# Kernel optimization log

Hardware: AMD Instinct MI355X
Metric: run time of the kernel (lower is better)

## Reference

```python
import jax, jax.numpy as jnp
import numpy as np

LMAX = 4
NCOEF = (LMAX + 1) ** 2  # 25 spherical-harmonic coefficients
EXPAND = np.repeat(np.arange(LMAX + 1), [2 * l + 1 for l in range(LMAX + 1)])  # per-l -> per-(l,m)
N, E, C, H, HEADS, ACH, VCH, F, G, DE, AEMB, MAXEL = 10000, 50000, 64, 64, 8, 16, 8, 128, 36, 32, 32, 100


def setup_inputs() -> dict:
    ks = jax.random.split(jax.random.key(0), 24)
    f = lambda i, shape, s=1.0: jax.random.normal(ks[i], shape, jnp.float32) * s
    return dict(
        x=f(0, (N, NCOEF, C)),
        edge_index=jax.random.randint(ks[1], (2, E), 0, N),
        atomic_numbers=jax.random.randint(ks[2], (N,), 0, MAXEL),
        edge_distance=jax.random.uniform(ks[3], (E, DE), jnp.float32),
        wigner=f(4, (E, NCOEF, NCOEF), 0.2),
        src_tab=f(5, (MAXEL, AEMB), 0.02), tgt_tab=f(6, (MAXEL, AEMB), 0.02),
        rad_w1=f(7, (DE + 2 * AEMB, 64), 0.1), rad_b1=jnp.zeros((64,), jnp.float32),
        rad_w2=f(8, (64, 64), 0.1), rad_b2=jnp.zeros((64,), jnp.float32),
        rad_w3=f(9, (64, (LMAX + 1) * 2 * C), 0.05), rad_b3=jnp.ones(((LMAX + 1) * 2 * C,), jnp.float32),
        W1=f(10, (2 * C, H), 0.05), W0_extra=f(11, (2 * C, HEADS * ACH + H), 0.05),
        alpha_dot=f(12, (HEADS, ACH), 0.1),
        to_grid=f(13, (G, NCOEF), 0.2), from_grid=f(14, (NCOEF, G), 0.2),
        proj_out=f(15, (HEADS * VCH, C), 0.1),
        gamma1=jnp.ones((C,), jnp.float32), gamma2=jnp.ones((C,), jnp.float32),
        gl_w=f(16, (C, F), 0.1), gl_b=jnp.zeros((F,), jnp.float32),
        ffn_w1=f(17, (C, F), 0.1), ffn_b1=jnp.zeros((F,), jnp.float32),
        ffn_w2=f(18, (F, C), 0.1), ffn_b2=jnp.zeros((C,), jnp.float32),
    )


def _rmsnorm(x, gamma, eps=1e-6):
    # equivariant norm over the coefficient axis, per node/channel
    rms = jnp.sqrt(jnp.mean(x * x, axis=1, keepdims=True) + eps)  # [N,1,C]
    return x / rms * gamma


def _s2_sep_act(gate, x, to_grid, from_grid):
    # separable S2 activation: scalars = silu(gating scalars); l>0 via grid SiLU
    grid = jnp.einsum('gi,nih->ngh', to_grid, x)
    xg = jnp.einsum('ig,ngh->nih', from_grid, jax.nn.silu(grid))
    return jnp.concatenate([jax.nn.silu(gate)[:, None, :], xg[:, 1:, :]], axis=1)


def reference(x, edge_index, atomic_numbers, edge_distance, wigner, src_tab, tgt_tab,
              rad_w1, rad_b1, rad_w2, rad_b2, rad_w3, rad_b3,
              W1, W0_extra, alpha_dot, to_grid, from_grid, proj_out,
              gamma1, gamma2, gl_w, gl_b, ffn_w1, ffn_b1, ffn_w2, ffn_b2):
    src, dst = edge_index[0], edge_index[1]
    # ---- SO2 equivariant graph attention (gather -> rotate -> conv -> act -> attn -> scatter) ----
    h = _rmsnorm(x, gamma1)
    xe = jnp.concatenate([h[src], h[dst]], axis=-1)          # [E,25,2C] edge gather
    xe = jnp.einsum('eij,ejc->eic', wigner, xe)              # rotate into edge frame
    ef = jnp.concatenate([edge_distance, src_tab[atomic_numbers[src]],
                          tgt_tab[atomic_numbers[dst]]], axis=-1)
    r = jax.nn.silu(ef @ rad_w1 + rad_b1)
    r = jax.nn.silu(r @ rad_w2 + rad_b2)
    r = (r @ rad_w3 + rad_b3).reshape(-1, LMAX + 1, 2 * C)[:, EXPAND, :]  # m-shared radial, [E,25,2C]
    xe = xe * r
    extra = xe[:, 0, :] @ W0_extra                           # extra m=0 channels
    alpha_f = extra[:, :HEADS * ACH].reshape(-1, HEADS, ACH)
    gate = extra[:, HEADS * ACH:]                            # [E,H]
    msg = jnp.einsum('eic,ch->eih', xe, W1)                  # [E,25,H]
    msg = _s2_sep_act(gate, msg, to_grid, from_grid)
    # attention weights: softmax over incoming edges of each destination node
    alpha = jnp.einsum('eha,ha->eh', jax.nn.silu(alpha_f), alpha_dot)
    amax = jax.lax.stop_gradient(jax.ops.segment_max(alpha, dst, num_segments=N))
    a = jnp.exp(alpha - amax[dst])
    a = a / (jax.ops.segment_sum(a, dst, num_segments=N)[dst] + 1e-8)
    msg = (msg.reshape(-1, NCOEF, HEADS, VCH) * a[:, None, :, None]).reshape(-1, NCOEF, HEADS * VCH)
    msg = jnp.einsum('eji,ejc->eic', wigner, msg)            # rotate back (D^T)
    agg = jax.ops.segment_sum(msg, dst, num_segments=N)      # scatter-add, [N,25,H]
    x = x + agg @ proj_out
    # ---- feed-forward with separable S2 activation ----
    h = _rmsnorm(x, gamma2)
    gate = h[:, 0, :] @ gl_w + gl_b
    f1 = jnp.einsum('nic,cf->nif', h, ffn_w1)
    f1 = jnp.concatenate([f1[:, :1, :] + ffn_b1, f1[:, 1:, :]], axis=1)  # bias on l=0 only
    f1 = _s2_sep_act(gate, f1, to_grid, from_grid)
    f2 = jnp.einsum('nif,fc->nic', f1, ffn_w2)
    f2 = jnp.concatenate([f2[:, :1, :] + ffn_b2, f2[:, 1:, :]], axis=1)
    return x + f2
```

## Files before the change

kernel.cpp:

```cpp
#include <hip/hip_runtime.h>
#include <hip/hip_bf16.h>

#define NN 10000
#define NE 50000
#define MAXDEG 32

typedef __attribute__((ext_vector_type(8))) short bfrag8;
typedef __attribute__((ext_vector_type(4))) short s16x4;
typedef __attribute__((ext_vector_type(8))) short s16x8;
typedef __attribute__((ext_vector_type(4))) float f32x4;

__device__ __forceinline__ float silu_f(float v){ return v / (1.0f + __expf(-v)); }
__device__ __forceinline__ short f2b(float f){
  unsigned u = __float_as_uint(f);
  u += 0x7fffu + ((u>>16)&1u);
  return (short)(u>>16);
}
__device__ __forceinline__ float b2f(short s){
  return __uint_as_float(((unsigned)(unsigned short)s)<<16);
}
__device__ __forceinline__ void gload_lds16(const void* g, void* l){
  __builtin_amdgcn_global_load_lds(
      (const __attribute__((address_space(1))) void*)g,
      (__attribute__((address_space(3))) void*)l, 16, 0, 0);
}

__global__ __launch_bounds__(256) void k_rms1(const float* __restrict__ x,
                                              const float* __restrict__ gamma,
                                              short* __restrict__ hT){
  int idx = blockIdx.x*256 + threadIdx.x;
  if (idx >= NN*64) return;
  int n = idx>>6, c = idx&63;
  const float* xp = x + (size_t)n*1600 + c;
  float v[25]; float ss = 0.f;
#pragma unroll
  for (int i=0;i<25;i++){ v[i] = xp[i*64]; ss += v[i]*v[i]; }
  float inv = gamma[c] * rsqrtf(ss*(1.f/25.f) + 1e-6f);
  short* hp = hT + (size_t)n*2048 + c*32;
  const int sw = (c>>1)&3;
#pragma unroll
  for (int s=0;s<4;s++){
    s16x8 o;
#pragma unroll
    for (int k=0;k<8;k++){
      int j = s*8 + k;
      o[k] = (j<25) ? f2b(v[j]*inv) : (short)0;
    }
    *(s16x8*)(hp + ((s ^ sw)<<3)) = o;
  }
}

__global__ void k_wprep(const float* __restrict__ W1, const float* __restrict__ tog,
                        const float* __restrict__ fromg, const float* __restrict__ proj,
                        const float* __restrict__ fw1, const float* __restrict__ fw2,
                        const float* __restrict__ rw1, const float* __restrict__ rw2,
                        const float* __restrict__ rw3, const float* __restrict__ w0e,
                        short* __restrict__ w1t, short* __restrict__ togA,
                        short* __restrict__ fgA, short* __restrict__ projT,
                        short* __restrict__ fw1T, short* __restrict__ fw2T,
                        short* __restrict__ rw1T, short* __restrict__ rw2T,
                        short* __restrict__ rw3T, short* __restrict__ w0eT){
  int t0 = blockIdx.x*blockDim.x + threadIdx.x;
  int stride = gridDim.x*blockDim.x;
  for (int idx=t0; idx<64*136; idx+=stride){
    int hh = idx/136, k = idx-136*hh;
    w1t[idx] = (k<128) ? f2b(W1[k*64+hh]) : (short)0;
  }
  for (int idx=t0; idx<48*40; idx+=stride){
    int g = idx/40, i = idx-40*g;
    togA[idx] = (g<36 && i<25) ? f2b(tog[g*25+i]) : (short)0;
  }
  for (int idx=t0; idx<32*72; idx+=stride){
    int j = idx/72, g = idx-72*j;
    fgA[idx] = (j<25 && g<36) ? f2b(fromg[j*36+g]) : (short)0;
  }
  for (int idx=t0; idx<64*64; idx+=stride){
    int c = idx>>6, k = idx&63;
    projT[idx] = f2b(proj[k*64+c]);
  }
  for (int idx=t0; idx<128*64; idx+=stride){
    int f = idx>>6, c = idx&63;
    fw1T[idx] = f2b(fw1[c*128+f]);
  }
  for (int idx=t0; idx<64*128; idx+=stride){
    int c = idx>>7, f = idx&127;
    fw2T[idx] = f2b(fw2[f*64+c]);
  }
  for (int idx=t0; idx<64*96; idx+=stride){
    int n = idx/96, k = idx-96*n;
    rw1T[idx] = f2b(rw1[k*64+n]);
  }
  for (int idx=t0; idx<64*64; idx+=stride){
    int n = idx>>6, k = idx&63;
    rw2T[idx] = f2b(rw2[k*64+n]);
  }
  for (int idx=t0; idx<640*64; idx+=stride){
    int n = idx>>6, k = idx&63;
    rw3T[idx] = f2b(rw3[(size_t)k*640+n]);
  }
  for (int idx=t0; idx<192*128; idx+=stride){
    int m = idx>>7, c = idx&127;
    w0eT[idx] = f2b(w0e[c*192+m]);
  }
}

__global__ __launch_bounds__(256) void k_fill(const int* __restrict__ ei,
                                              int* __restrict__ cnt,
                                              unsigned short* __restrict__ eidTab){
  int e = blockIdx.x*256 + threadIdx.x;
  if (e >= NE) return;
  int dst = ei[NE+e];
  int pos = atomicAdd(&cnt[dst], 1);
  if (pos < MAXDEG) eidTab[dst*MAXDEG + pos] = (unsigned short)e;
}

__global__ __launch_bounds__(256) void k_scan(const int* __restrict__ cnt,
                                              int* __restrict__ pref){
  __shared__ int ts[256];
  int tid = threadIdx.x;
  int base = tid*40;
  int s = 0;
  for (int k=0;k<40;k++){ int i = base+k; if (i<NN) s += min(cnt[i],MAXDEG); }
  ts[tid] = s;
  __syncthreads();
  if (tid==0){ int run=0; for(int t=0;t<256;t++){ int v=ts[t]; ts[t]=run; run+=v; } }
  __syncthreads();
  int run = ts[tid];
  for (int k=0;k<40;k++){
    int i = base+k;
    if (i<NN){ pref[i]=run; run += min(cnt[i],MAXDEG); }
  }
}

__global__ __launch_bounds__(256) void k_compact(const int* __restrict__ cnt,
                                                 const int* __restrict__ pref,
                                                 const unsigned short* __restrict__ eidTab,
                                                 int* __restrict__ order){
  int idx = blockIdx.x*256 + threadIdx.x;
  if (idx >= NN*MAXDEG) return;
  int n = idx>>5, k = idx&31;
  if (k < min(cnt[n],MAXDEG)) order[pref[n]+k] = (int)eidTab[n*MAXDEG+k];
}

__global__ __launch_bounds__(256,4) void k_radial(
  const int* __restrict__ ei, const int* __restrict__ an,
  const float* __restrict__ edist,
  const float* __restrict__ stab, const float* __restrict__ ttab,
  const short* __restrict__ rw1T, const float* __restrict__ rb1,
  const short* __restrict__ rw2T, const float* __restrict__ rb2,
  const short* __restrict__ rw3T, const float* __restrict__ rb3,
  short* __restrict__ rfS)
{
  __shared__ __align__(16) short SP[7936];
  const int tid = threadIdx.x;
  const int wv = tid>>6, lane = tid&63, lo = lane&15, q = lane>>4;
  const int e0 = blockIdx.x*32;
  {
    int e = tid>>3;
    int ee = min(e0+e, NE-1);
    int srcE = ei[ee], dstE = ei[NE+ee];
    const float* dp = edist + (size_t)ee*32;
    const float* sp = stab + (size_t)an[srcE]*32;
    const float* tp = ttab + (size_t)an[dstE]*32;
    int kb = tid&7;
#pragma unroll
    for (int it=0; it<12; ++it){
      int k = kb + it*8;
      float v = (k<32) ? dp[k] : (k<64 ? sp[k-32] : tp[k-64]);
      SP[e*104+k] = f2b(v);
    }
  }
  __syncthreads();
  {
    f32x4 zf={0.f,0.f,0.f,0.f}; f32x4 acc[2]={zf,zf};
#pragma unroll
    for (int kt=0;kt<3;kt++){
      bfrag8 a = *(const bfrag8*)&rw1T[(wv*16+lo)*96 + kt*32 + q*8];
#pragma unroll
      for (int et=0;et<2;et++){
        bfrag8 b = *(const bfrag8*)&SP[(et*16+lo)*104 + kt*32 + q*8];
        acc[et] = __builtin_amdgcn_mfma_f32_16x16x32_bf16(a,b,acc[et],0,0,0);
      }
    }
    int n1 = wv*16 + q*4;
    const float4 bb = *(const float4*)&rb1[n1];
#pragma unroll
    for (int et=0;et<2;et++){
      s16x4 o;
      o[0]=f2b(silu_f(acc[et][0]+bb.x)); o[1]=f2b(silu_f(acc[et][1]+bb.y));
      o[2]=f2b(silu_f(acc[et][2]+bb.z)); o[3]=f2b(silu_f(acc[et][3]+bb.w));
      *(s16x4*)&SP[3328 + (et*16+lo)*72 + n1] = o;
    }
  }
  __syncthreads();
  {
    f32x4 zf={0.f,0.f,0.f,0.f}; f32x4 acc[2]={zf,zf};
#pragma unroll
    for (int kt=0;kt<2;kt++){
      bfrag8 a = *(const bfrag8*)&rw2T[(wv*16+lo)*64 + kt*32 + q*8];
#pragma unroll
      for (int et=0;et<2;et++){
        bfrag8 b = *(const bfrag8*)&SP[3328 + (et*16+lo)*72 + kt*32 + q*8];
        acc[et] = __builtin_amdgcn_mfma_f32_16x16x32_bf16(a,b,acc[et],0,0,0);
      }
    }
    int n2 = wv*16 + q*4;
    const float4 bb = *(const float4*)&rb2[n2];
#pragma unroll
    for (int et=0;et<2;et++){
      s16x4 o;
      o[0]=f2b(silu_f(acc[et][0]+bb.x)); o[1]=f2b(silu_f(acc[et][1]+bb.y));
      o[2]=f2b(silu_f(acc[et][2]+bb.z)); o[3]=f2b(silu_f(acc[et][3]+bb.w));
      *(s16x4*)&SP[5632 + (et*16+lo)*72 + n2] = o;
    }
  }
  __syncthreads();
  {
    bfrag8 bfr[2][2];
#pragma unroll
    for (int et=0;et<2;et++)
#pragma unroll
      for (int kt=0;kt<2;kt++)
        bfr[et][kt] = *(const bfrag8*)&SP[5632 + (et*16+lo)*72 + kt*32 + q*8];
    for (int mi=0; mi<10; ++mi){
      int n3base = (wv + mi*4)*16;
      f32x4 zf={0.f,0.f,0.f,0.f}; f32x4 acc[2]={zf,zf};
#pragma unroll
      for (int kt=0;kt<2;kt++){
        bfrag8 a = *(const bfrag8*)&rw3T[(size_t)(n3base+lo)*64 + kt*32 + q*8];
        acc[0] = __builtin_amdgcn_mfma_f32_16x16x32_bf16(a,bfr[0][kt],acc[0],0,0,0);
        acc[1] = __builtin_amdgcn_mfma_f32_16x16x32_bf16(a,bfr[1][kt],acc[1],0,0,0);
      }
      int n3 = n3base + q*4;
      const float4 bb = *(const float4*)&rb3[n3];
#pragma unroll
      for (int et=0;et<2;et++){
        int e = e0 + et*16 + lo;
        if (e < NE){
          s16x4 o;
          o[0]=f2b(acc[et][0]+bb.x); o[1]=f2b(acc[et][1]+bb.y);
          o[2]=f2b(acc[et][2]+bb.z); o[3]=f2b(acc[et][3]+bb.w);
          *(s16x4*)&rfS[(size_t)e*640 + n3] = o;
        }
      }
    }
  }
}

__global__ __launch_bounds__(256,8) void k_edge(
  const short* __restrict__ hT, const int* __restrict__ ei,
  const int* __restrict__ order, const float* __restrict__ wig,
  const short* __restrict__ w1t, const short* __restrict__ togA,
  const short* __restrict__ fgA, const short* __restrict__ w0eT,
  const float* __restrict__ adot,
  const short* __restrict__ rfS, float* __restrict__ asum,
  float* __restrict__ agg)
{
  __shared__ __align__(16) short SH[7312];
  float* gateL = (float*)&SH[7168];
  float* ahead = (float*)&SH[7296];
  const int tid = threadIdx.x;
  const int wv = tid>>6, lane = tid&63, lo = lane&15, q = lane>>4;
  const int bid = blockIdx.x;
  const int e = order[(bid&7)*(NE/8) + (bid>>3)];
  const int src = ei[e], dst = ei[NE+e];

  {
    const char* g0 = (const char*)(hT + (size_t)src*2048) + wv*1024 + lane*16;
    const char* g1 = (const char*)(hT + (size_t)dst*2048) + wv*1024 + lane*16;
    gload_lds16(g0, (char*)SH + wv*1024);
    gload_lds16(g1, (char*)SH + 4096 + wv*1024);
  }
  {
    const s16x4 z4 = {0,0,0,0};
    if (tid < 128) *(s16x4*)&SH[4096 + tid*4] = z4;
  }
  const float* w = wig + (size_t)e*625;
  const bfrag8 wz = {0,0,0,0,0,0,0,0};
  bfrag8 wb0, wtb0, wb1 = wz, wtb1 = wz;
#pragma unroll
  for (int m=0;m<8;m++){
    int j = q*8+m;
    float v0  = (j<25) ? w[lo*25+j] : 0.f;
    float vt0 = (j<25) ? w[j*25+lo] : 0.f;
    wb0[m]  = f2b(v0);
    wtb0[m] = f2b(vt0);
  }
  if (lo < 9){
#pragma unroll
    for (int m=0;m<8;m++){
      int j = q*8+m;
      float v1  = (j<25) ? w[(16+lo)*25+j]  : 0.f;
      float vt1 = (j<25) ? w[j*25+16+lo]    : 0.f;
      wb1[m]  = f2b(v1);
      wtb1[m] = f2b(vt1);
    }
  }
  s16x4 rvp[2][2];
  {
    const short* rrow = rfS + (size_t)e*640;
#pragma unroll
    for (int t=0;t<2;t++){
      int c0 = (2*wv+t)*16 + q*4;
#pragma unroll
      for (int nt=0;nt<2;nt++){
        int i = nt*16 + lo;
        int l = (i>=16)?4:((i>=9)?3:((i>=4)?2:((i>=1)?1:0)));
        rvp[t][nt] = *(const s16x4*)&rrow[l*128 + c0];
      }
    }
  }
  asm volatile("s_waitcnt vmcnt(0)" ::: "memory");
  __syncthreads();

  f32x4 xacc[2][2];
  {
    const f32x4 zf = {0.f,0.f,0.f,0.f};
#pragma unroll
    for (int t=0;t<2;t++){
      int c = (2*wv+t)*16 + lo;
      bfrag8 a = *(const bfrag8*)&SH[c*32 + ((q ^ ((c>>1)&3))<<3)];
      xacc[t][0] = __builtin_amdgcn_mfma_f32_16x16x32_bf16(a, wb0, zf, 0,0,0);
      xacc[t][1] = __builtin_amdgcn_mfma_f32_16x16x32_bf16(a, wb1, zf, 0,0,0);
    }
  }
  __syncthreads();
#pragma unroll
  for (int t=0;t<2;t++){
    int c0 = (2*wv+t)*16 + q*4;
#pragma unroll
    for (int nt=0;nt<2;nt++){
      int i = nt*16 + lo;
      s16x4 rv = rvp[t][nt];
      s16x4 o;
#pragma unroll
      for (int r=0;r<4;r++) o[r] = f2b(xacc[t][nt][r]*b2f(rv[r]));
      *(s16x4*)&SH[i*136 + c0] = o;
    }
  }
  __syncthreads();

  {
    bfrag8 xb[4];
#pragma unroll
    for (int kt=0;kt<4;kt++) xb[kt] = *(const bfrag8*)&SH[kt*32 + q*8];
    const f32x4 zf = {0.f,0.f,0.f,0.f};
#pragma unroll
    for (int t=0;t<3;t++){
      const int mt = wv*3 + t;
      f32x4 acc = zf;
#pragma unroll
      for (int kt=0;kt<4;kt++){
        bfrag8 a = *(const bfrag8*)&w0eT[(mt*16+lo)*128 + kt*32 + q*8];
        acc = __builtin_amdgcn_mfma_f32_16x16x32_bf16(a, xb[kt], acc, 0,0,0);
      }
      if (mt < 8){
        float s = 0.f;
#pragma unroll
        for (int r=0;r<4;r++) s += silu_f(acc[r]) * adot[mt*16 + q*4 + r];
        s += __shfl_xor(s, 16);
        s += __shfl_xor(s, 32);
        float eh = __expf(s);
        if (lane==0){
          ahead[mt] = eh;
          unsafeAtomicAdd(&asum[(size_t)dst*8 + mt], eh);
        }
      } else if (lo==0){
        int g0 = mt*16 - 128 + q*4;
#pragma unroll
        for (int r=0;r<4;r++) gateL[g0+r] = silu_f(acc[r]);
      }
    }
  }
  {
    const int hh = wv*16 + lo;
    const f32x4 zf = {0.f,0.f,0.f,0.f};
    f32x4 acc[2] = {zf,zf};
#pragma unroll
    for (int kt=0;kt<4;kt++){
      bfrag8 b = *(const bfrag8*)&w1t[hh*136 + kt*32 + q*8];
#pragma unroll
      for (int t=0;t<2;t++){
        bfrag8 a = *(const bfrag8*)&SH[(t*16+lo)*136 + kt*32 + q*8];
        acc[t] = __builtin_amdgcn_mfma_f32_16x16x32_bf16(a, b, acc[t], 0,0,0);
      }
    }
#pragma unroll
    for (int t=0;t<2;t++){
      s16x4 o;
#pragma unroll
      for (int r=0;r<4;r++) o[r] = f2b(acc[t][r]);
      *(s16x4*)&SH[4608 + hh*40 + t*16 + q*4] = o;
    }
  }
  __syncthreads();

  {
    const int hh = wv*16 + lo;
    bfrag8 b = *(const bfrag8*)&SH[4608 + hh*40 + q*8];
    const f32x4 zf = {0.f,0.f,0.f,0.f};
    f32x4 acc[3] = {zf,zf,zf};
#pragma unroll
    for (int t=0;t<3;t++){
      bfrag8 a = *(const bfrag8*)&togA[(t*16+lo)*40 + q*8];
      acc[t] = __builtin_amdgcn_mfma_f32_16x16x32_bf16(a, b, acc[t], 0,0,0);
    }
#pragma unroll
    for (int t=0;t<3;t++){
      s16x4 o;
#pragma unroll
      for (int r=0;r<4;r++) o[r] = f2b(silu_f(acc[t][r]));
      *(s16x4*)&SH[hh*72 + t*16 + q*4] = o;
    }
  }
  {
    const int hh = wv*16 + lo;
    const f32x4 zf = {0.f,0.f,0.f,0.f};
    f32x4 acc[2] = {zf,zf};
#pragma unroll
    for (int kt=0;kt<2;kt++){
      bfrag8 b = *(const bfrag8*)&SH[hh*72 + kt*32 + q*8];
#pragma unroll
      for (int t=0;t<2;t++){
        bfrag8 a = *(const bfrag8*)&fgA[(t*16+lo)*72 + kt*32 + q*8];
        acc[t] = __builtin_amdgcn_mfma_f32_16x16x32_bf16(a, b, acc[t], 0,0,0);
      }
    }
    float ah = ahead[hh>>3];
#pragma unroll
    for (int t=0;t<2;t++){
      s16x4 o;
#pragma unroll
      for (int r=0;r<4;r++){
        int j = t*16 + q*4 + r;
        float v = (j==0) ? gateL[hh] : acc[t][r];
        o[r] = f2b(v*ah);
      }
      *(s16x4*)&SH[4608 + hh*40 + t*16 + q*4] = o;
    }
  }
  {
    const int hh = wv*16 + lo;
    bfrag8 b = *(const bfrag8*)&SH[4608 + hh*40 + q*8];
    const f32x4 zf = {0.f,0.f,0.f,0.f};
    f32x4 acc0 = __builtin_amdgcn_mfma_f32_16x16x32_bf16(wtb0, b, zf, 0,0,0);
    f32x4 acc1 = __builtin_amdgcn_mfma_f32_16x16x32_bf16(wtb1, b, zf, 0,0,0);
    float* aggp = agg + (size_t)dst*1600;
#pragma unroll
    for (int r=0;r<4;r++){
      int i0 = q*4 + r;
      unsafeAtomicAdd(&aggp[i0*64 + hh], acc0[r]);
      int i1 = 16 + q*4 + r;
      if (i1 < 25) unsafeAtomicAdd(&aggp[i1*64 + hh], acc1[r]);
    }
  }
}

__global__ __launch_bounds__(256,4) void k_node(
  const float* __restrict__ x, const float* __restrict__ aggin,
  const float* __restrict__ asum,
  const short* __restrict__ projT, const float* __restrict__ gamma2,
  const float* __restrict__ glw, const float* __restrict__ glb,
  const short* __restrict__ fw1T, const float* __restrict__ fb1,
  const short* __restrict__ fw2T, const float* __restrict__ fb2,
  const short* __restrict__ togA, const short* __restrict__ fgA,
  float* __restrict__ out)
{
  __shared__ __align__(16) short P[19072];
  float* xF    = (float*)P;
  short* sgB   = P + 4352;
  short* hh2B  = P + 4352;
  short* f1B   = P + 13568;
  short* aggB  = P + 13568;
  short* xgB   = P + 13568;
  float* invc  = ((float*)P) + 9344;
  float* gateF = ((float*)P) + 9408;
  const int tid = threadIdx.x;
  const int wv = tid>>6, lane = tid&63, lo = lane&15, q = lane>>4;
  const int n = blockIdx.x;
  const s16x4 z4 = {0,0,0,0};

  for (int idx=tid; idx<400; idx+=256){
    int i = idx>>4, k = idx&15;
    float sc = 1.f/(asum[(size_t)n*8 + (k>>1)] + 1e-8f);
    const float4 v = *(const float4*)(aggin + (size_t)n*1600 + (size_t)idx*4);
    s16x4 o; o[0]=f2b(v.x*sc); o[1]=f2b(v.y*sc); o[2]=f2b(v.z*sc); o[3]=f2b(v.w*sc);
    *(s16x4*)&aggB[i*72 + k*4] = o;
  }
  for (int idx=tid; idx<126; idx+=256)
    *(s16x4*)&hh2B[25*72 + idx*4] = z4;
  for (int idx=tid; idx<512; idx+=256){
    int f = idx>>2, gg = 48 + (idx&3)*4;
    *(s16x4*)&sgB[f*72 + gg] = z4;
  }
  __syncthreads();

  {
    f32x4 zf={0.f,0.f,0.f,0.f}; f32x4 acc[2]={zf,zf};
    const int c = wv*16 + lo;
#pragma unroll
    for (int kt=0;kt<2;kt++){
      bfrag8 b = *(const bfrag8*)&projT[c*64 + kt*32 + q*8];
#pragma unroll
      for (int t=0;t<2;t++){
        bfrag8 a = *(const bfrag8*)&aggB[(t*16+lo)*72 + kt*32 + q*8];
        acc[t] = __builtin_amdgcn_mfma_f32_16x16x32_bf16(a,b,acc[t],0,0,0);
      }
    }
#pragma unroll
    for (int t=0;t<2;t++)
#pragma unroll
      for (int r=0;r<4;r++){
        int i = t*16 + q*4 + r;
        if (i<25) xF[i*68+c] = acc[t][r] + x[(size_t)n*1600 + i*64 + c];
      }
  }
  __syncthreads();
  if (tid<64){
    float ss=0.f;
#pragma unroll
    for (int i=0;i<25;i++){ float v = xF[i*68+tid]; ss += v*v; }
    invc[tid] = gamma2[tid]*rsqrtf(ss*(1.f/25.f)+1e-6f);
  }
  __syncthreads();
  for (int idx=tid; idx<1600; idx+=256){
    int i=idx>>6, c=idx&63;
    hh2B[i*72+c] = f2b(xF[i*68+c]*invc[c]);
  }
  if (tid<128){
    float a = glb[tid];
#pragma unroll 8
    for (int c=0;c<64;c++) a += xF[c]*invc[c]*glw[c*128+tid];
    gateF[tid] = silu_f(a);
  }
  __syncthreads();

  {
    f32x4 zf={0.f,0.f,0.f,0.f}; f32x4 acc[2][2]={{zf,zf},{zf,zf}};
#pragma unroll
    for (int kt=0;kt<2;kt++){
      bfrag8 a0 = *(const bfrag8*)&hh2B[(lo)*72 + kt*32 + q*8];
      bfrag8 a1 = *(const bfrag8*)&hh2B[(16+lo)*72 + kt*32 + q*8];
#pragma unroll
      for (int s=0;s<2;s++){
        int f = wv*32 + s*16 + lo;
        bfrag8 b = *(const bfrag8*)&fw1T[f*64 + kt*32 + q*8];
        acc[0][s] = __builtin_amdgcn_mfma_f32_16x16x32_bf16(a0,b,acc[0][s],0,0,0);
        acc[1][s] = __builtin_amdgcn_mfma_f32_16x16x32_bf16(a1,b,acc[1][s],0,0,0);
      }
    }
#pragma unroll
    for (int s=0;s<2;s++){
      int f = wv*32 + s*16 + lo;
      float bb = fb1[f];
#pragma unroll
      for (int t=0;t<2;t++){
        s16x4 o;
#pragma unroll
        for (int r=0;r<4;r++){
          int i = t*16+q*4+r;
          o[r] = f2b(acc[t][s][r] + (i==0 ? bb : 0.f));
        }
        *(s16x4*)&f1B[f*40 + t*16 + q*4] = o;
      }
    }
  }
  __syncthreads();

  {
    f32x4 zf={0.f,0.f,0.f,0.f}; f32x4 acc[3][2]={{zf,zf},{zf,zf},{zf,zf}};
    bfrag8 a0 = *(const bfrag8*)&togA[(lo)*40 + q*8];
    bfrag8 a1 = *(const bfrag8*)&togA[(16+lo)*40 + q*8];
    bfrag8 a2 = *(const bfrag8*)&togA[(32+lo)*40 + q*8];
#pragma unroll
    for (int s=0;s<2;s++){
      int f = wv*32 + s*16 + lo;
      bfrag8 b = *(const bfrag8*)&f1B[f*40 + q*8];
      acc[0][s] = __builtin_amdgcn_mfma_f32_16x16x32_bf16(a0,b,acc[0][s],0,0,0);
      acc[1][s] = __builtin_amdgcn_mfma_f32_16x16x32_bf16(a1,b,acc[1][s],0,0,0);
      acc[2][s] = __builtin_amdgcn_mfma_f32_16x16x32_bf16(a2,b,acc[2][s],0,0,0);
    }
#pragma unroll
    for (int s=0;s<2;s++){
      int f = wv*32 + s*16 + lo;
#pragma unroll
      for (int t=0;t<3;t++){
        s16x4 o;
#pragma unroll
        for (int r=0;r<4;r++) o[r] = f2b(silu_f(acc[t][s][r]));
        *(s16x4*)&sgB[f*72 + t*16 + q*4] = o;
      }
    }
  }
  __syncthreads();

  {
    f32x4 zf={0.f,0.f,0.f,0.f}; f32x4 acc[2][2]={{zf,zf},{zf,zf}};
#pragma unroll
    for (int kt=0;kt<2;kt++){
#pragma unroll
      for (int t=0;t<2;t++){
        bfrag8 b = *(const bfrag8*)&fgA[(t*16+lo)*72 + kt*32 + q*8];
#pragma unroll
        for (int s=0;s<2;s++){
          bfrag8 a = *(const bfrag8*)&sgB[(wv*32+s*16+lo)*72 + kt*32 + q*8];
          acc[s][t] = __builtin_amdgcn_mfma_f32_16x16x32_bf16(a,b,acc[s][t],0,0,0);
        }
      }
    }
#pragma unroll
    for (int s=0;s<2;s++){
      int f0 = wv*32 + s*16 + q*4;
#pragma unroll
      for (int t=0;t<2;t++){
        int j = t*16 + lo;
        s16x4 o;
#pragma unroll
        for (int r=0;r<4;r++)
          o[r] = f2b(j==0 ? gateF[f0+r] : acc[s][t][r]);
        *(s16x4*)&xgB[j*136 + f0] = o;
      }
    }
  }
  __syncthreads();

  {
    f32x4 zf={0.f,0.f,0.f,0.f}; f32x4 acc[2]={zf,zf};
    const int c = wv*16 + lo;
#pragma unroll
    for (int kt=0;kt<4;kt++){
      bfrag8 b = *(const bfrag8*)&fw2T[c*128 + kt*32 + q*8];
#pragma unroll
      for (int t=0;t<2;t++){
        bfrag8 a = *(const bfrag8*)&xgB[(t*16+lo)*136 + kt*32 + q*8];
        acc[t] = __builtin_amdgcn_mfma_f32_16x16x32_bf16(a,b,acc[t],0,0,0);
      }
    }
    float bb = fb2[c];
#pragma unroll
    for (int t=0;t<2;t++)
#pragma unroll
      for (int r=0;r<4;r++){
        int i = t*16 + q*4 + r;
        if (i<25)
          out[(size_t)n*1600 + i*64 + c] = xF[i*68+c] + acc[t][r] + (i==0 ? bb : 0.f);
      }
  }
}

extern "C" void kernel_launch(void* const* d_in, const int* in_sizes, int n_in,
                              void* d_out, int out_size, void* d_ws, size_t ws_size,
                              hipStream_t stream) {
  (void)in_sizes; (void)n_in; (void)ws_size;
  const float* x     = (const float*)d_in[0];
  const int*   ei    = (const int*)d_in[1];
  const int*   an    = (const int*)d_in[2];
  const float* edist = (const float*)d_in[3];
  const float* wig   = (const float*)d_in[4];
  const float* stab  = (const float*)d_in[5];
  const float* ttab  = (const float*)d_in[6];
  const float* rw1   = (const float*)d_in[7];
  const float* rb1   = (const float*)d_in[8];
  const float* rw2   = (const float*)d_in[9];
  const float* rb2   = (const float*)d_in[10];
  const float* rw3   = (const float*)d_in[11];
  const float* rb3   = (const float*)d_in[12];
  const float* W1    = (const float*)d_in[13];
  const float* w0e   = (const float*)d_in[14];
  const float* adot  = (const float*)d_in[15];
  const float* tog   = (const float*)d_in[16];
  const float* fromg = (const float*)d_in[17];
  const float* proj  = (const float*)d_in[18];
  const float* g1    = (const float*)d_in[19];
  const float* g2    = (const float*)d_in[20];
  const float* glw   = (const float*)d_in[21];
  const float* glb   = (const float*)d_in[22];
  const float* fw1   = (const float*)d_in[23];
  const float* fb1   = (const float*)d_in[24];
  const float* fw2   = (const float*)d_in[25];
  const float* fb2   = (const float*)d_in[26];
  float* out = (float*)d_out;

  char* wsb = (char*)d_ws;
  short* hT     = (short*)(wsb);
  short* rfS    = (short*)(wsb + 40960000);
  float* asum   = (float*)(wsb + 104960000);
  int*   cnt    = (int*)(wsb + 105280000);
  int*   pref   = (int*)(wsb + 105320000);
  int*   order  = (int*)(wsb + 105360000);
  unsigned short* eidTab = (unsigned short*)(wsb + 105560000);
  short* w1t    = (short*)(wsb + 106200000);
  short* togA   = (short*)(wsb + 106217408);
  short* fgA    = (short*)(wsb + 106221248);
  short* projT  = (short*)(wsb + 106225856);
  short* fw1T   = (short*)(wsb + 106234048);
  short* fw2T   = (short*)(wsb + 106250432);
  short* rw1T   = (short*)(wsb + 106266816);
  short* rw2T   = (short*)(wsb + 106279104);
  short* rw3T   = (short*)(wsb + 106287296);
  short* w0eT   = (short*)(wsb + 106369216);

  hipMemsetAsync(asum, 0, (size_t)NN*8*sizeof(float), stream);
  hipMemsetAsync(cnt, 0, (size_t)NN*sizeof(int), stream);
  hipMemsetAsync(d_out, 0, (size_t)out_size*sizeof(float), stream);

  k_wprep<<<32, 256, 0, stream>>>(W1, tog, fromg, proj, fw1, fw2, rw1, rw2, rw3, w0e,
                                  w1t, togA, fgA, projT, fw1T, fw2T,
                                  rw1T, rw2T, rw3T, w0eT);
  k_fill   <<<(NE+255)/256, 256, 0, stream>>>(ei, cnt, eidTab);
  k_scan   <<<1, 256, 0, stream>>>(cnt, pref);
  k_compact<<<(NN*MAXDEG+255)/256, 256, 0, stream>>>(cnt, pref, eidTab, order);
  k_rms1  <<<(NN*64+255)/256, 256, 0, stream>>>(x, g1, hT);
  k_radial<<<(NE+31)/32, 256, 0, stream>>>(ei, an, edist, stab, ttab,
                                           rw1T, rb1, rw2T, rb2, rw3T, rb3, rfS);
  k_edge  <<<NE, 256, 0, stream>>>(hT, ei, order, wig, w1t, togA, fgA, w0eT, adot,
                                   rfS, asum, out);
  k_node  <<<NN, 256, 0, stream>>>(x, out, asum, projT, g2, glw, glb,
                                   fw1T, fb1, fw2T, fb2, togA, fgA, out);
}
```

Baseline: 1.083 ms.

## Process edges per destination node to replace atomic scatter with register accumulation

The edge kernel now launches one block per destination node and loops serially over that node's incoming edges from the bucket table. It accumulates the rotated messages in MFMA registers and the softmax denominators in LDS, then writes each aggregate row once with normalization applied. This drops the scan and compact kernels, the output and softmax-sum memsets, and all global float atomics. In exchange, the per-edge work inside each block is serialized with several barriers per edge. The dst row load is now shared across edges, and load imbalance across nodes of different degree becomes possible. Occupancy is reduced to 6 blocks because of the larger LDS footprint.

Result: slower. 1.280 ms (+18.1%).

```diff
diff --git a/kernel.cpp b/kernel.cpp
--- a/kernel.cpp
+++ b/kernel.cpp
@@ -114,34 +114,6 @@
   if (pos < MAXDEG) eidTab[dst*MAXDEG + pos] = (unsigned short)e;
 }
 
-__global__ __launch_bounds__(256) void k_scan(const int* __restrict__ cnt,
-                                              int* __restrict__ pref){
-  __shared__ int ts[256];
-  int tid = threadIdx.x;
-  int base = tid*40;
-  int s = 0;
-  for (int k=0;k<40;k++){ int i = base+k; if (i<NN) s += min(cnt[i],MAXDEG); }
-  ts[tid] = s;
-  __syncthreads();
-  if (tid==0){ int run=0; for(int t=0;t<256;t++){ int v=ts[t]; ts[t]=run; run+=v; } }
-  __syncthreads();
-  int run = ts[tid];
-  for (int k=0;k<40;k++){
-    int i = base+k;
-    if (i<NN){ pref[i]=run; run += min(cnt[i],MAXDEG); }
-  }
-}
-
-__global__ __launch_bounds__(256) void k_compact(const int* __restrict__ cnt,
-                                                 const int* __restrict__ pref,
-                                                 const unsigned short* __restrict__ eidTab,
-                                                 int* __restrict__ order){
-  int idx = blockIdx.x*256 + threadIdx.x;
-  if (idx >= NN*MAXDEG) return;
-  int n = idx>>5, k = idx&31;
-  if (k < min(cnt[n],MAXDEG)) order[pref[n]+k] = (int)eidTab[n*MAXDEG+k];
-}
-
 __global__ __launch_bounds__(256,4) void k_radial(
   const int* __restrict__ ei, const int* __restrict__ an,
   const float* __restrict__ edist,
@@ -247,218 +219,229 @@
   }
 }
 
-__global__ __launch_bounds__(256,8) void k_edge(
+__global__ __launch_bounds__(256,6) void k_edge(
   const short* __restrict__ hT, const int* __restrict__ ei,
-  const int* __restrict__ order, const float* __restrict__ wig,
+  const float* __restrict__ wig,
+  const int* __restrict__ cnt, const unsigned short* __restrict__ eidTab,
   const short* __restrict__ w1t, const short* __restrict__ togA,
   const short* __restrict__ fgA, const short* __restrict__ w0eT,
   const float* __restrict__ adot,
-  const short* __restrict__ rfS, float* __restrict__ asum,
-  float* __restrict__ agg)
+  const short* __restrict__ rfS, float* __restrict__ agg)
 {
-  __shared__ __align__(16) short SH[7312];
-  float* gateL = (float*)&SH[7168];
-  float* ahead = (float*)&SH[7296];
+  __shared__ __align__(16) short SH[11424];
+  float* wigL  = (float*)&SH[8704];
+  float* gateL = (float*)&SH[11264];
+  float* ahead = (float*)&SH[11392];
+  float* dsum  = (float*)&SH[11408];
   const int tid = threadIdx.x;
   const int wv = tid>>6, lane = tid&63, lo = lane&15, q = lane>>4;
-  const int bid = blockIdx.x;
-  const int e = order[(bid&7)*(NE/8) + (bid>>3)];
-  const int src = ei[e], dst = ei[NE+e];
-
-  {
-    const char* g0 = (const char*)(hT + (size_t)src*2048) + wv*1024 + lane*16;
-    const char* g1 = (const char*)(hT + (size_t)dst*2048) + wv*1024 + lane*16;
-    gload_lds16(g0, (char*)SH + wv*1024);
-    gload_lds16(g1, (char*)SH + 4096 + wv*1024);
-  }
+  const int n = blockIdx.x;
+  const int deg = min(cnt[n], MAXDEG);
+  const bfrag8 wz = {0,0,0,0,0,0,0,0};
+
   {
     const s16x4 z4 = {0,0,0,0};
-    if (tid < 128) *(s16x4*)&SH[4096 + tid*4] = z4;
-  }
-  const float* w = wig + (size_t)e*625;
-  const bfrag8 wz = {0,0,0,0,0,0,0,0};
-  bfrag8 wb0, wtb0, wb1 = wz, wtb1 = wz;
-#pragma unroll
-  for (int m=0;m<8;m++){
-    int j = q*8+m;
-    float v0  = (j<25) ? w[lo*25+j] : 0.f;
-    float vt0 = (j<25) ? w[j*25+lo] : 0.f;
-    wb0[m]  = f2b(v0);
-    wtb0[m] = f2b(vt0);
-  }
-  if (lo < 9){
+    for (int idx=tid; idx<1152; idx+=256) *(s16x4*)&SH[4096 + idx*4] = z4;
+    if (tid < 8) dsum[tid] = 0.f;
+  }
+  gload_lds16((const char*)(hT + (size_t)n*2048) + wv*1024 + lane*16,
+              (char*)SH + 4096 + wv*1024);
+
+  f32x4 aca0 = {0.f,0.f,0.f,0.f}, aca1 = {0.f,0.f,0.f,0.f};
+
+  for (int k=0; k<deg; ++k){
+    const int e = (int)eidTab[n*MAXDEG + k];
+    const int src = ei[e];
+    gload_lds16((const char*)(hT + (size_t)src*2048) + wv*1024 + lane*16,
+                (char*)SH + wv*1024);
+    {
+      const float* w = wig + (size_t)e*625;
+      for (int idx=tid; idx<625; idx+=256) wigL[idx] = w[idx];
+    }
+    s16x4 rvp[2][2];
+    {
+      const short* rrow = rfS + (size_t)e*640;
+#pragma unroll
+      for (int t=0;t<2;t++){
+        int c0 = (2*wv+t)*16 + q*4;
+#pragma unroll
+        for (int nt=0;nt<2;nt++){
+          int i = nt*16 + lo;
+          int l = (i>=16)?4:((i>=9)?3:((i>=4)?2:((i>=1)?1:0)));
+          rvp[t][nt] = *(const s16x4*)&rrow[l*128 + c0];
+        }
+      }
+    }
+    asm volatile("s_waitcnt vmcnt(0)" ::: "memory");
+    __syncthreads();
+
+    bfrag8 wb0, wtb0, wb1 = wz, wtb1 = wz;
 #pragma unroll
     for (int m=0;m<8;m++){
       int j = q*8+m;
-      float v1  = (j<25) ? w[(16+lo)*25+j]  : 0.f;
-      float vt1 = (j<25) ? w[j*25+16+lo]    : 0.f;
-      wb1[m]  = f2b(v1);
-      wtb1[m] = f2b(vt1);
-    }
-  }
-  s16x4 rvp[2][2];
-  {
-    const short* rrow = rfS + (size_t)e*640;
+      wb0[m]  = (j<25) ? f2b(wigL[lo*25+j]) : (short)0;
+      wtb0[m] = (j<25) ? f2b(wigL[j*25+lo]) : (short)0;
+    }
+    if (lo < 9){
+#pragma unroll
+      for (int m=0;m<8;m++){
+        int j = q*8+m;
+        wb1[m]  = (j<25) ? f2b(wigL[(16+lo)*25+j]) : (short)0;
+        wtb1[m] = (j<25) ? f2b(wigL[j*25+16+lo])   : (short)0;
+      }
+    }
+    f32x4 xacc[2][2];
+    {
+      const f32x4 zf = {0.f,0.f,0.f,0.f};
+#pragma unroll
+      for (int t=0;t<2;t++){
+        int c = (2*wv+t)*16 + lo;
+        bfrag8 a = *(const bfrag8*)&SH[c*32 + ((q ^ ((c>>1)&3))<<3)];
+        xacc[t][0] = __builtin_amdgcn_mfma_f32_16x16x32_bf16(a, wb0, zf, 0,0,0);
+        xacc[t][1] = __builtin_amdgcn_mfma_f32_16x16x32_bf16(a, wb1, zf, 0,0,0);
+      }
+    }
+    __syncthreads();
 #pragma unroll
     for (int t=0;t<2;t++){
       int c0 = (2*wv+t)*16 + q*4;
 #pragma unroll
       for (int nt=0;nt<2;nt++){
         int i = nt*16 + lo;
-        int l = (i>=16)?4:((i>=9)?3:((i>=4)?2:((i>=1)?1:0)));
-        rvp[t][nt] = *(const s16x4*)&rrow[l*128 + c0];
-      }
-    }
-  }
-  asm volatile("s_waitcnt vmcnt(0)" ::: "memory");
-  __syncthreads();
-
-  f32x4 xacc[2][2];
-  {
-    const f32x4 zf = {0.f,0.f,0.f,0.f};
-#pragma unroll
-    for (int t=0;t<2;t++){
-      int c = (2*wv+t)*16 + lo;
-      bfrag8 a = *(const bfrag8*)&SH[c*32 + ((q ^ ((c>>1)&3))<<3)];
-      xacc[t][0] = __builtin_amdgcn_mfma_f32_16x16x32_bf16(a, wb0, zf, 0,0,0);
-      xacc[t][1] = __builtin_amdgcn_mfma_f32_16x16x32_bf16(a, wb1, zf, 0,0,0);
-    }
-  }
-  __syncthreads();
-#pragma unroll
-  for (int t=0;t<2;t++){
-    int c0 = (2*wv+t)*16 + q*4;
-#pragma unroll
-    for (int nt=0;nt<2;nt++){
-      int i = nt*16 + lo;
-      s16x4 rv = rvp[t][nt];
-      s16x4 o;
-#pragma unroll
-      for (int r=0;r<4;r++) o[r] = f2b(xacc[t][nt][r]*b2f(rv[r]));
-      *(s16x4*)&SH[i*136 + c0] = o;
-    }
-  }
-  __syncthreads();
-
-  {
-    bfrag8 xb[4];
-#pragma unroll
-    for (int kt=0;kt<4;kt++) xb[kt] = *(const bfrag8*)&SH[kt*32 + q*8];
-    const f32x4 zf = {0.f,0.f,0.f,0.f};
-#pragma unroll
-    for (int t=0;t<3;t++){
-      const int mt = wv*3 + t;
-      f32x4 acc = zf;
+        s16x4 rv = rvp[t][nt];
+        s16x4 o;
+#pragma unroll
+        for (int r=0;r<4;r++) o[r] = f2b(xacc[t][nt][r]*b2f(rv[r]));
+        *(s16x4*)&SH[4096 + i*136 + c0] = o;
+      }
+    }
+    __syncthreads();
+
+    {
+      bfrag8 xb[4];
+#pragma unroll
+      for (int kt=0;kt<4;kt++) xb[kt] = *(const bfrag8*)&SH[4096 + kt*32 + q*8];
+      const f32x4 zf = {0.f,0.f,0.f,0.f};
+#pragma unroll
+      for (int t=0;t<3;t++){
+        const int mt = wv*3 + t;
+        f32x4 acc = zf;
+#pragma unroll
+        for (int kt=0;kt<4;kt++){
+          bfrag8 a = *(const bfrag8*)&w0eT[(mt*16+lo)*128 + kt*32 + q*8];
+          acc = __builtin_amdgcn_mfma_f32_16x16x32_bf16(a, xb[kt], acc, 0,0,0);
+        }
+        if (mt < 8){
+          float s = 0.f;
+#pragma unroll
+          for (int r=0;r<4;r++) s += silu_f(acc[r]) * adot[mt*16 + q*4 + r];
+          s += __shfl_xor(s, 16);
+          s += __shfl_xor(s, 32);
+          float eh = __expf(s);
+          if (lane==0){
+            ahead[mt] = eh;
+            dsum[mt] += eh;
+          }
+        } else if (lo==0){
+          int g0 = mt*16 - 128 + q*4;
+#pragma unroll
+          for (int r=0;r<4;r++) gateL[g0+r] = silu_f(acc[r]);
+        }
+      }
+    }
+    {
+      const int hh = wv*16 + lo;
+      const f32x4 zf = {0.f,0.f,0.f,0.f};
+      f32x4 acc[2] = {zf,zf};
 #pragma unroll
       for (int kt=0;kt<4;kt++){
-        bfrag8 a = *(const bfrag8*)&w0eT[(mt*16+lo)*128 + kt*32 + q*8];
-        acc = __builtin_amdgcn_mfma_f32_16x16x32_bf16(a, xb[kt], acc, 0,0,0);
-      }
-      if (mt < 8){
-        float s = 0.f;
-#pragma unroll
-        for (int r=0;r<4;r++) s += silu_f(acc[r]) * adot[mt*16 + q*4 + r];
-        s += __shfl_xor(s, 16);
-        s += __shfl_xor(s, 32);
-        float eh = __expf(s);
-        if (lane==0){
-          ahead[mt] = eh;
-          unsafeAtomicAdd(&asum[(size_t)dst*8 + mt], eh);
-        }
-      } else if (lo==0){
-        int g0 = mt*16 - 128 + q*4;
-#pragma unroll
-        for (int r=0;r<4;r++) gateL[g0+r] = silu_f(acc[r]);
-      }
-    }
-  }
+        bfrag8 b = *(const bfrag8*)&w1t[hh*136 + kt*32 + q*8];
+#pragma unroll
+        for (int t=0;t<2;t++){
+          bfrag8 a = *(const bfrag8*)&SH[4096 + (t*16+lo)*136 + kt*32 + q*8];
+          acc[t] = __builtin_amdgcn_mfma_f32_16x16x32_bf16(a, b, acc[t], 0,0,0);
+        }
+      }
+#pragma unroll
+      for (int t=0;t<2;t++){
+        s16x4 o;
+#pragma unroll
+        for (int r=0;r<4;r++) o[r] = f2b(acc[t][r]);
+        *(s16x4*)&SH[8704 + hh*40 + t*16 + q*4] = o;
+      }
+    }
+    __syncthreads();
+
+    {
+      const int hh = wv*16 + lo;
+      bfrag8 b = *(const bfrag8*)&SH[8704 + hh*40 + q*8];
+      const f32x4 zf = {0.f,0.f,0.f,0.f};
+      f32x4 acc[3] = {zf,zf,zf};
+#pragma unroll
+      for (int t=0;t<3;t++){
+        bfrag8 a = *(const bfrag8*)&togA[(t*16+lo)*40 + q*8];
+        acc[t] = __builtin_amdgcn_mfma_f32_16x16x32_bf16(a, b, acc[t], 0,0,0);
+      }
+#pragma unroll
+      for (int t=0;t<3;t++){
+        s16x4 o;
+#pragma unroll
+        for (int r=0;r<4;r++) o[r] = f2b(silu_f(acc[t][r]));
+        *(s16x4*)&SH[4096 + hh*72 + t*16 + q*4] = o;
+      }
+    }
+    {
+      const int hh = wv*16 + lo;
+      const f32x4 zf = {0.f,0.f,0.f,0.f};
+      f32x4 acc[2] = {zf,zf};
+#pragma unroll
+      for (int kt=0;kt<2;kt++){
+        bfrag8 b = *(const bfrag8*)&SH[4096 + hh*72 + kt*32 + q*8];
+#pragma unroll
+        for (int t=0;t<2;t++){
+          bfrag8 a = *(const bfrag8*)&fgA[(t*16+lo)*72 + kt*32 + q*8];
+          acc[t] = __builtin_amdgcn_mfma_f32_16x16x32_bf16(a, b, acc[t], 0,0,0);
+        }
+      }
+      float ah = ahead[hh>>3];
+#pragma unroll
+      for (int t=0;t<2;t++){
+        s16x4 o;
+#pragma unroll
+        for (int r=0;r<4;r++){
+          int j = t*16 + q*4 + r;
+          float v = (j==0) ? gateL[hh] : acc[t][r];
+          o[r] = f2b(v*ah);
+        }
+        *(s16x4*)&SH[8704 + hh*40 + t*16 + q*4] = o;
+      }
+    }
+    {
+      const int hh = wv*16 + lo;
+      bfrag8 b = *(const bfrag8*)&SH[8704 + hh*40 + q*8];
+      aca0 = __builtin_amdgcn_mfma_f32_16x16x32_bf16(wtb0, b, aca0, 0,0,0);
+      aca1 = __builtin_amdgcn_mfma_f32_16x16x32_bf16(wtb1, b, aca1, 0,0,0);
+    }
+    __syncthreads();
+  }
+
+  __syncthreads();
   {
     const int hh = wv*16 + lo;
-    const f32x4 zf = {0.f,0.f,0.f,0.f};
-    f32x4 acc[2] = {zf,zf};
-#pragma unroll
-    for (int kt=0;kt<4;kt++){
-      bfrag8 b = *(const bfrag8*)&w1t[hh*136 + kt*32 + q*8];
-#pragma unroll
-      for (int t=0;t<2;t++){
-        bfrag8 a = *(const bfrag8*)&SH[(t*16+lo)*136 + kt*32 + q*8];
-        acc[t] = __builtin_amdgcn_mfma_f32_16x16x32_bf16(a, b, acc[t], 0,0,0);
-      }
-    }
-#pragma unroll
-    for (int t=0;t<2;t++){
-      s16x4 o;
-#pragma unroll
-      for (int r=0;r<4;r++) o[r] = f2b(acc[t][r]);
-      *(s16x4*)&SH[4608 + hh*40 + t*16 + q*4] = o;
-    }
-  }
-  __syncthreads();
-
-  {
-    const int hh = wv*16 + lo;
-    bfrag8 b = *(const bfrag8*)&SH[4608 + hh*40 + q*8];
-    const f32x4 zf = {0.f,0.f,0.f,0.f};
-    f32x4 acc[3] = {zf,zf,zf};
-#pragma unroll
-    for (int t=0;t<3;t++){
-      bfrag8 a = *(const bfrag8*)&togA[(t*16+lo)*40 + q*8];
-      acc[t] = __builtin_amdgcn_mfma_f32_16x16x32_bf16(a, b, acc[t], 0,0,0);
-    }
-#pragma unroll
-    for (int t=0;t<3;t++){
-      s16x4 o;
-#pragma unroll
-      for (int r=0;r<4;r++) o[r] = f2b(silu_f(acc[t][r]));
-      *(s16x4*)&SH[hh*72 + t*16 + q*4] = o;
-    }
-  }
-  {
-    const int hh = wv*16 + lo;
-    const f32x4 zf = {0.f,0.f,0.f,0.f};
-    f32x4 acc[2] = {zf,zf};
-#pragma unroll
-    for (int kt=0;kt<2;kt++){
-      bfrag8 b = *(const bfrag8*)&SH[hh*72 + kt*32 + q*8];
-#pragma unroll
-      for (int t=0;t<2;t++){
-        bfrag8 a = *(const bfrag8*)&fgA[(t*16+lo)*72 + kt*32 + q*8];
-        acc[t] = __builtin_amdgcn_mfma_f32_16x16x32_bf16(a, b, acc[t], 0,0,0);
-      }
-    }
-    float ah = ahead[hh>>3];
-#pragma unroll
-    for (int t=0;t<2;t++){
-      s16x4 o;
-#pragma unroll
-      for (int r=0;r<4;r++){
-        int j = t*16 + q*4 + r;
-        float v = (j==0) ? gateL[hh] : acc[t][r];
-        o[r] = f2b(v*ah);
-      }
-      *(s16x4*)&SH[4608 + hh*40 + t*16 + q*4] = o;
-    }
-  }
-  {
-    const int hh = wv*16 + lo;
-    bfrag8 b = *(const bfrag8*)&SH[4608 + hh*40 + q*8];
-    const f32x4 zf = {0.f,0.f,0.f,0.f};
-    f32x4 acc0 = __builtin_amdgcn_mfma_f32_16x16x32_bf16(wtb0, b, zf, 0,0,0);
-    f32x4 acc1 = __builtin_amdgcn_mfma_f32_16x16x32_bf16(wtb1, b, zf, 0,0,0);
-    float* aggp = agg + (size_t)dst*1600;
+    float sc = 1.f/(dsum[hh>>3] + 1e-8f);
+    float* aggp = agg + (size_t)n*1600;
 #pragma unroll
     for (int r=0;r<4;r++){
       int i0 = q*4 + r;
-      unsafeAtomicAdd(&aggp[i0*64 + hh], acc0[r]);
+      aggp[i0*64 + hh] = aca0[r]*sc;
       int i1 = 16 + q*4 + r;
-      if (i1 < 25) unsafeAtomicAdd(&aggp[i1*64 + hh], acc1[r]);
+      if (i1 < 25) aggp[i1*64 + hh] = aca1[r]*sc;
     }
   }
 }
 
 __global__ __launch_bounds__(256,4) void k_node(
   const float* __restrict__ x, const float* __restrict__ aggin,
-  const float* __restrict__ asum,
   const short* __restrict__ projT, const float* __restrict__ gamma2,
   const float* __restrict__ glw, const float* __restrict__ glb,
   const short* __restrict__ fw1T, const float* __restrict__ fb1,
@@ -482,9 +465,8 @@
 
   for (int idx=tid; idx<400; idx+=256){
     int i = idx>>4, k = idx&15;
-    float sc = 1.f/(asum[(size_t)n*8 + (k>>1)] + 1e-8f);
     const float4 v = *(const float4*)(aggin + (size_t)n*1600 + (size_t)idx*4);
-    s16x4 o; o[0]=f2b(v.x*sc); o[1]=f2b(v.y*sc); o[2]=f2b(v.z*sc); o[3]=f2b(v.w*sc);
+    s16x4 o; o[0]=f2b(v.x); o[1]=f2b(v.y); o[2]=f2b(v.z); o[3]=f2b(v.w);
     *(s16x4*)&aggB[i*72 + k*4] = o;
   }
   for (int idx=tid; idx<126; idx+=256)
@@ -651,7 +633,7 @@
 extern "C" void kernel_launch(void* const* d_in, const int* in_sizes, int n_in,
                               void* d_out, int out_size, void* d_ws, size_t ws_size,
                               hipStream_t stream) {
-  (void)in_sizes; (void)n_in; (void)ws_size;
+  (void)in_sizes; (void)n_in; (void)ws_size; (void)out_size;
   const float* x     = (const float*)d_in[0];
   const int*   ei    = (const int*)d_in[1];
   const int*   an    = (const int*)d_in[2];
@@ -684,37 +666,30 @@
   char* wsb = (char*)d_ws;
   short* hT     = (short*)(wsb);
   short* rfS    = (short*)(wsb + 40960000);
-  float* asum   = (float*)(wsb + 104960000);
-  int*   cnt    = (int*)(wsb + 105280000);
-  int*   pref   = (int*)(wsb + 105320000);
-  int*   order  = (int*)(wsb + 105360000);
-  unsigned short* eidTab = (unsigned short*)(wsb + 105560000);
-  short* w1t    = (short*)(wsb + 106200000);
-  short* togA   = (short*)(wsb + 106217408);
-  short* fgA    = (short*)(wsb + 106221248);
-  short* projT  = (short*)(wsb + 106225856);
-  short* fw1T   = (short*)(wsb + 106234048);
-  short* fw2T   = (short*)(wsb + 106250432);
-  short* rw1T   = (short*)(wsb + 106266816);
-  short* rw2T   = (short*)(wsb + 106279104);
-  short* rw3T   = (short*)(wsb + 106287296);
-  short* w0eT   = (short*)(wsb + 106369216);
-
-  hipMemsetAsync(asum, 0, (size_t)NN*8*sizeof(float), stream);
+  int*   cnt    = (int*)(wsb + 104960000);
+  unsigned short* eidTab = (unsigned short*)(wsb + 105000000);
+  short* w1t    = (short*)(wsb + 105640000);
+  short* togA   = (short*)(wsb + 105657408);
+  short* fgA    = (short*)(wsb + 105661248);
+  short* projT  = (short*)(wsb + 105665856);
+  short* fw1T   = (short*)(wsb + 105674048);
+  short* fw2T   = (short*)(wsb + 105690432);
+  short* rw1T   = (short*)(wsb + 105706816);
+  short* rw2T   = (short*)(wsb + 105719104);
+  short* rw3T   = (short*)(wsb + 105727296);
+  short* w0eT   = (short*)(wsb + 105809216);
+
   hipMemsetAsync(cnt, 0, (size_t)NN*sizeof(int), stream);
-  hipMemsetAsync(d_out, 0, (size_t)out_size*sizeof(float), stream);
 
   k_wprep<<<32, 256, 0, stream>>>(W1, tog, fromg, proj, fw1, fw2, rw1, rw2, rw3, w0e,
                                   w1t, togA, fgA, projT, fw1T, fw2T,
                                   rw1T, rw2T, rw3T, w0eT);
-  k_fill   <<<(NE+255)/256, 256, 0, stream>>>(ei, cnt, eidTab);
-  k_scan   <<<1, 256, 0, stream>>>(cnt, pref);
-  k_compact<<<(NN*MAXDEG+255)/256, 256, 0, stream>>>(cnt, pref, eidTab, order);
+  k_fill  <<<(NE+255)/256, 256, 0, stream>>>(ei, cnt, eidTab);
   k_rms1  <<<(NN*64+255)/256, 256, 0, stream>>>(x, g1, hT);
   k_radial<<<(NE+31)/32, 256, 0, stream>>>(ei, an, edist, stab, ttab,
                                            rw1T, rb1, rw2T, rb2, rw3T, rb3, rfS);
-  k_edge  <<<NE, 256, 0, stream>>>(hT, ei, order, wig, w1t, togA, fgA, w0eT, adot,
-                                   rfS, asum, out);
-  k_node  <<<NN, 256, 0, stream>>>(x, out, asum, projT, g2, glw, glb,
+  k_edge  <<<NN, 256, 0, stream>>>(hT, ei, wig, cnt, eidTab,
+                                   w1t, togA, fgA, w0eT, adot, rfS, out);
+  k_node  <<<NN, 256, 0, stream>>>(x, out, projT, g2, glw, glb,
                                    fw1T, fb1, fw2T, fb2, togA, fgA, out);
 }
```
